# Kernel tuning notes

Measured on AMD Instinct MI355X. Metric: run time of the kernel, lower is better.

The kernel has to match this reference:

```python
import jax, jax.numpy as jnp
import numpy as np

N_STATE = 16
PNAMES = ['in_w', 'conv_w', 'conv_b', 'xproj_w', 'dt_w', 'dt_b', 'A_log', 'D', 'ln_g', 'ln_b', 'out_w']


def _ss2d_params(key, dm, K):
    di = 2 * dm                       # expand = 2
    dr = (dm + 15) // 16              # dt_rank = ceil(d_model/16)
    ks = jax.random.split(key, 6)
    s = lambda k, shape, sc: jax.random.normal(k, shape, jnp.float32) * sc
    cshape = (di, 1, 3, 3) if K == 4 else (di, 1, 3)   # depthwise conv kernel
    return {
        'in_w': s(ks[0], (2 * di, dm), dm ** -0.5),
        'conv_w': s(ks[1], cshape, 0.3),
        'conv_b': jnp.zeros((di,), jnp.float32),
        'xproj_w': s(ks[2], (K, dr + 2 * N_STATE, di), di ** -0.5),
        'dt_w': s(ks[3], (K, di, dr), dr ** -0.5),
        'dt_b': s(ks[4], (K, di), 0.1),
        'A_log': jnp.log(jnp.arange(1, N_STATE + 1, dtype=jnp.float32)) * jnp.ones((K, di, N_STATE), jnp.float32),
        'D': jnp.ones((K, di), jnp.float32),
        'ln_g': jnp.ones((di,), jnp.float32),
        'ln_b': jnp.zeros((di,), jnp.float32),
        'out_w': s(ks[5], (dm, di), di ** -0.5),
    }


def _ln(x, g, b, eps=1e-5):
    m = jnp.mean(x, -1, keepdims=True)
    v = jnp.mean((x - m) ** 2, -1, keepdims=True)
    return (x - m) * jax.lax.rsqrt(v + eps) * g + b


def _scan_branches(xs, p):
    # xs: (B, K, di, L) -- selective scan along L for each direction k
    dr = p['dt_w'].shape[-1]
    x_dbl = jnp.einsum('bkdl,kcd->bkcl', xs, p['xproj_w'])
    dts, Bs, Cs = jnp.split(x_dbl, [dr, dr + N_STATE], axis=2)
    delta = jax.nn.softplus(jnp.einsum('bkrl,kdr->bkdl', dts, p['dt_w']) + p['dt_b'][None, :, :, None])
    A = -jnp.exp(p['A_log'])                               # (K, di, N)
    dA = jnp.exp(jnp.einsum('bkdl,kdn->lbkdn', delta, A))  # time-major for scan
    dBu = jnp.einsum('bkdl,bknl,bkdl->lbkdn', delta, Bs, xs)

    def step(h, io):
        a, bu = io
        h = a * h + bu
        return h, h

    h0 = jnp.zeros(dA.shape[1:], xs.dtype)
    _, hs = jax.lax.scan(step, h0, (dA, dBu))              # (L, B, K, di, N)
    y = jnp.einsum('lbkdn,bknl->bkdl', hs, Cs)
    return y + xs * p['D'][None, :, :, None]


def _ss2d_2d(x, p):
    # VMamba SS2D: x (B, H, W, dm) -> (B, H, W, dm), 4 scan directions
    xz = jnp.einsum('bhwc,ec->bhwe', x, p['in_w'])
    xin, z = jnp.split(xz, 2, -1)
    u = xin.transpose(0, 3, 1, 2)
    u = jax.lax.conv_general_dilated(u, p['conv_w'], (1, 1), 'SAME',
        dimension_numbers=('NCHW', 'OIHW', 'NCHW'), feature_group_count=u.shape[1])
    u = jax.nn.silu(u + p['conv_b'][None, :, None, None])
    Bb, di, H, W = u.shape
    L = H * W
    xf = u.reshape(Bb, di, L)                              # row-major
    xt = u.transpose(0, 1, 3, 2).reshape(Bb, di, L)        # col-major
    xs = jnp.stack([xf, xt, xf[..., ::-1], xt[..., ::-1]], 1)
    ys = _scan_branches(xs, p)                             # (B, 4, di, L)
    y0 = ys[:, 0]
    y2 = ys[:, 2][..., ::-1]
    y1 = ys[:, 1].reshape(Bb, di, W, H).transpose(0, 1, 3, 2).reshape(Bb, di, L)
    y3 = ys[:, 3][..., ::-1].reshape(Bb, di, W, H).transpose(0, 1, 3, 2).reshape(Bb, di, L)
    y = (y0 + y1 + y2 + y3).transpose(0, 2, 1).reshape(Bb, H, W, di)
    y = _ln(y, p['ln_g'], p['ln_b']) * jax.nn.silu(z)
    return jnp.einsum('bhwe,ce->bhwc', y, p['out_w'])


def _ss2d_1d(x, p):
    # SS2D_xb fuse block: x (B, L, dm) -> (B, L, dm), bidirectional 1D scan
    xz = jnp.einsum('blc,ec->ble', x, p['in_w'])
    xin, z = jnp.split(xz, 2, -1)
    u = xin.transpose(0, 2, 1)
    u = jax.lax.conv_general_dilated(u, p['conv_w'], (1,), 'SAME',
        dimension_numbers=('NCH', 'OIH', 'NCH'), feature_group_count=u.shape[1])
    u = jax.nn.silu(u + p['conv_b'][None, :, None])
    xs = jnp.stack([u, u[..., ::-1]], 1)                   # K = 2
    ys = _scan_branches(xs, p)
    y = (ys[:, 0] + ys[:, 1][..., ::-1]).transpose(0, 2, 1)
    y = _ln(y, p['ln_g'], p['ln_b']) * jax.nn.silu(z)
    return jnp.einsum('ble,ce->blc', y, p['out_w'])


def _bridge(C1, C2, C3, p1, p2, p3, pf, n1_g, n1_b):
    y1 = _ss2d_2d(C1.transpose(0, 2, 3, 1), p1).transpose(0, 3, 1, 2)
    y2 = _ss2d_2d(C2.transpose(0, 2, 3, 1), p2).transpose(0, 3, 1, 2)
    y3 = _ss2d_2d(C3.transpose(0, 2, 3, 1), p3).transpose(0, 3, 1, 2)
    B_, C, H, W = y1.shape                                 # C=24, H=W=112
    # faithful RAW reshapes (no permute), exactly as the torch source does
    F1 = y1.reshape(B_, H * W, C)
    F2 = y2.reshape(B_, H * W // 2, C)
    F3 = y3.reshape(B_, H * W // 4, C)
    F = jnp.concatenate([F1, F2, F3], axis=1)              # (B, 21952, 24)
    F = F + _ss2d_1d(_ln(F, n1_g, n1_b), pf)               # dropout = identity (eval)
    o1 = F[:, :12544, :].reshape(B_, C, H, W)
    o2 = F[:, 12544:18816, :].reshape(B_, C * 2, H // 2, W // 2)
    o3 = F[:, 18816:, :].reshape(B_, C * 4, H // 4, W // 4)
    return (o1, o2, o3)


def setup_inputs() -> dict:
    key = jax.random.key(0)
    ks = jax.random.split(key, 7)
    inp = {
        'C1': jax.random.normal(ks[0], (1, 24, 112, 112), jnp.float32),
        'C2': jax.random.normal(ks[1], (1, 48, 56, 56), jnp.float32),
        'C3': jax.random.normal(ks[2], (1, 96, 28, 28), jnp.float32),
    }
    for pfx, dm, K, kk in [('m1', 24, 4, ks[3]), ('m2', 48, 4, ks[4]), ('m3', 96, 4, ks[5]), ('fz', 24, 2, ks[6])]:
        p = _ss2d_params(kk, dm, K)
        for n in PNAMES:
            inp[pfx + '_' + n] = p[n]
    inp['n1_g'] = jnp.ones((24,), jnp.float32)
    inp['n1_b'] = jnp.zeros((24,), jnp.float32)
    return inp


def reference(C1, C2, C3, m1_in_w, m1_conv_w, m1_conv_b, m1_xproj_w, m1_dt_w, m1_dt_b, m1_A_log, m1_D, m1_ln_g, m1_ln_b, m1_out_w, m2_in_w, m2_conv_w, m2_conv_b, m2_xproj_w, m2_dt_w, m2_dt_b, m2_A_log, m2_D, m2_ln_g, m2_ln_b, m2_out_w, m3_in_w, m3_conv_w, m3_conv_b, m3_xproj_w, m3_dt_w, m3_dt_b, m3_A_log, m3_D, m3_ln_g, m3_ln_b, m3_out_w, fz_in_w, fz_conv_w, fz_conv_b, fz_xproj_w, fz_dt_w, fz_dt_b, fz_A_log, fz_D, fz_ln_g, fz_ln_b, fz_out_w, n1_g, n1_b):
    p1 = dict(zip(PNAMES, (m1_in_w, m1_conv_w, m1_conv_b, m1_xproj_w, m1_dt_w, m1_dt_b, m1_A_log, m1_D, m1_ln_g, m1_ln_b, m1_out_w)))
    p2 = dict(zip(PNAMES, (m2_in_w, m2_conv_w, m2_conv_b, m2_xproj_w, m2_dt_w, m2_dt_b, m2_A_log, m2_D, m2_ln_g, m2_ln_b, m2_out_w)))
    p3 = dict(zip(PNAMES, (m3_in_w, m3_conv_w, m3_conv_b, m3_xproj_w, m3_dt_w, m3_dt_b, m3_A_log, m3_D, m3_ln_g, m3_ln_b, m3_out_w)))
    pf = dict(zip(PNAMES, (fz_in_w, fz_conv_w, fz_conv_b, fz_xproj_w, fz_dt_w, fz_dt_b, fz_A_log, fz_D, fz_ln_g, fz_ln_b, fz_out_w)))
    return _bridge(C1, C2, C3, p1, p2, p3, pf, n1_g, n1_b)
```

## Files before the change

kernel.cpp:

```cpp
#include <hip/hip_runtime.h>
#include <hip/hip_bf16.h>
#include <hip/hip_fp16.h>

#define NST 16
#define L2E 1.4426950408889634f

typedef const void* inp;
typedef __half h16;

struct Job {
  inp Cin;
  inp in_w, conv_w, conv_b, xproj_w, dt_w, dt_b, A_log, D, ln_g, ln_b, out_w;
  h16 *u_pre, *z, *u, *delta, *Bs, *Cs, *yg;
  h16 *Hc;
  float *yacc, *Wc, *bc, *Ssum, *A2t, *F0out;
  float *outF; const float* resid;
  const int* aflg;
  int dm, di, dr, K, H, W, L, NCH, CLEN, is2d, TL, CG, PT, cinf;
};
struct Jobs { Job j[4]; int n; const int* dtf; };

__device__ __forceinline__ float ldw(inp p, size_t i, int f32){
  return f32 ? ((const float*)p)[i]
             : __bfloat162float(((const __hip_bfloat16*)p)[i]);
}
__device__ __forceinline__ float hf(const h16* p, size_t i){ return __half2float(p[i]); }
__device__ __forceinline__ float sigm(float x){ return 1.0f/(1.0f + __expf(-x)); }
__device__ __forceinline__ float silu_(float x){ return x * sigm(x); }
__device__ __forceinline__ float softp(float x){ return (x > 20.0f) ? x : __logf(1.0f + __expf(x)); }

__device__ __forceinline__ int map_pos(const Job& J, int k, int l){
  int rev   = J.is2d ? (k >= 2) : (k == 1);
  int trans = J.is2d ? (k & 1) : 0;
  int sl = rev ? (J.L - 1 - l) : l;
  return trans ? ((sl % J.H)*J.W + sl / J.H) : sl;
}

union F4H { float4 f; __half2 h[4]; };

__device__ __forceinline__ void ld16v(const h16* p, float* o){
  const float4* q = (const float4*)p;
  F4H a, b; a.f = q[0]; b.f = q[1];
  #pragma unroll
  for (int i = 0; i < 4; i++){ float2 x = __half22float2(a.h[i]); o[2*i] = x.x; o[2*i+1] = x.y; }
  #pragma unroll
  for (int i = 0; i < 4; i++){ float2 x = __half22float2(b.h[i]); o[8+2*i] = x.x; o[8+2*i+1] = x.y; }
}

__device__ __forceinline__ void ld8v(const h16* p, float* o){
  F4H a; a.f = *(const float4*)p;
  #pragma unroll
  for (int i = 0; i < 4; i++){ float2 x = __half22float2(a.h[i]); o[2*i] = x.x; o[2*i+1] = x.y; }
}


__global__ void k_detect(const unsigned* D1, int* flag){
  if (threadIdx.x == 0 && blockIdx.x == 0)
    flag[0] = (D1[0] == 0x3F800000u) ? 1 : 0;
}

__global__ void k_wcomb(Jobs js){
  int f32 = *js.dtf;
  int b = blockIdx.x;
  for (int m = 0; m < js.n; m++){
    const Job& J = js.j[m];
    int CC = J.di + 2*NST;
    int CC2 = CC + NST;
    int tot = J.K * CC2 * J.di;
    int nb = (tot + 255) >> 8;
    if (b < nb){
      int t = (b << 8) + (int)threadIdx.x;
      if (t < tot){
        int d = t % J.di; int r = t / J.di; int cout = r % CC2; int k = r / CC2;
        if (cout < J.di){
          float v = 0.0f;
          for (int rr = 0; rr < J.dr; rr++)
            v += ldw(J.dt_w, (size_t)(k*J.di + cout)*J.dr + rr, f32) *
                 ldw(J.xproj_w, (size_t)(k*(J.dr + 2*NST) + rr)*J.di + d, f32);
          J.Wc[(size_t)(k*CC + cout)*J.di + d] = v;
          if (d == 0) J.bc[k*CC + cout] = ldw(J.dt_b, k*J.di + cout, f32);
        } else if (cout < CC){
          int nn = cout - J.di;
          J.Wc[(size_t)(k*CC + cout)*J.di + d] =
            ldw(J.xproj_w, (size_t)(k*(J.dr + 2*NST) + J.dr + nn)*J.di + d, f32);
          if (d == 0) J.bc[k*CC + cout] = 0.0f;
        } else {
          int nn = cout - CC;
          J.A2t[(size_t)(k*NST + nn)*J.di + d] =
            -L2E*__expf(ldw(J.A_log, ((size_t)(k*J.di + d) << 4) + nn, f32));
        }
      }
      return;
    }
    b -= nb;
  }
}

__global__ void k_chkA(Jobs js, int* afl){
  int m = blockIdx.x;
  if (m >= js.n) return;
  const Job& J = js.j[m];
  __shared__ int ok;
  if (threadIdx.x == 0) ok = 1;
  __syncthreads();
  int tot = J.K * NST * J.di;
  int bad = 0;
  for (int t = threadIdx.x; t < tot; t += 256){
    int d = t % J.di; int r = t / J.di; int n = r % NST; int k = r / NST;
    float base = J.A2t[(size_t)(k*NST + 0)*J.di + d];
    float v    = J.A2t[(size_t)(k*NST + n)*J.di + d];
    float expect = (float)(n+1)*base;
    if (fabsf(v - expect) > 1e-4f*fabsf(expect) + 1e-6f) bad = 1;
  }
  if (bad) ok = 0;
  __syncthreads();
  if (threadIdx.x == 0) afl[m] = ok;
}

__global__ void k_inproj(Jobs js){
  int f32 = *js.dtf;
  int b = blockIdx.x;
  for (int m = 0; m < js.n; m++){
    const Job& J = js.j[m];
    int tot = 2*J.di*J.L;
    int nb = (tot + 255) >> 8;
    if (b < nb){
      int cf = J.cinf ? 1 : f32;
      int t = (b << 8) + (int)threadIdx.x;
      if (t < tot){
        int p = t % J.L; int e = t / J.L;
        float acc;
        if (cf && f32){
          const float* Ci = (const float*)J.Cin;
          const float4* w4 = (const float4*)((const float*)J.in_w + (size_t)e*J.dm);
          float a0 = 0.f, a1 = 0.f, a2 = 0.f, a3 = 0.f;
          int n4 = J.dm >> 2;
          for (int c4 = 0; c4 < n4; c4++){
            float4 w = w4[c4];
            int c = c4 << 2;
            a0 = fmaf(Ci[(size_t)(c+0)*J.L + p], w.x, a0);
            a1 = fmaf(Ci[(size_t)(c+1)*J.L + p], w.y, a1);
            a2 = fmaf(Ci[(size_t)(c+2)*J.L + p], w.z, a2);
            a3 = fmaf(Ci[(size_t)(c+3)*J.L + p], w.w, a3);
          }
          acc = (a0+a1)+(a2+a3);
        } else {
          float a0 = 0.f, a1 = 0.f, a2 = 0.f, a3 = 0.f;
          for (int c = 0; c < J.dm; c += 4){
            a0 = fmaf(ldw(J.Cin, (size_t)(c+0)*J.L + p, cf), ldw(J.in_w, (size_t)e*J.dm + c+0, f32), a0);
            a1 = fmaf(ldw(J.Cin, (size_t)(c+1)*J.L + p, cf), ldw(J.in_w, (size_t)e*J.dm + c+1, f32), a1);
            a2 = fmaf(ldw(J.Cin, (size_t)(c+2)*J.L + p, cf), ldw(J.in_w, (size_t)e*J.dm + c+2, f32), a2);
            a3 = fmaf(ldw(J.Cin, (size_t)(c+3)*J.L + p, cf), ldw(J.in_w, (size_t)e*J.dm + c+3, f32), a3);
          }
          acc = (a0+a1)+(a2+a3);
        }
        if (e < J.di) J.u_pre[(size_t)p*J.di + e] = __float2half(acc);
        else          J.z[(size_t)p*J.di + (e - J.di)] = __float2half(acc);
      }
      return;
    }
    b -= nb;
  }
}

__global__ void k_conv(Jobs js){
  int f32 = *js.dtf;
  int b = blockIdx.x;
  for (int m = 0; m < js.n; m++){
    const Job& J = js.j[m];
    int tot = J.L * J.di;
    int nb = (tot + 255) >> 8;
    if (b < nb){
      int t = (b << 8) + (int)threadIdx.x;
      if (t < tot){
        int d = t % J.di; int p = t / J.di;
        float acc = ldw(J.conv_b, d, f32);
        if (J.is2d){
          int h = p / J.W, w = p % J.W;
          for (int kh = 0; kh < 3; kh++){
            int hh = h + kh - 1;
            if ((unsigned)hh < (unsigned)J.H){
              for (int kw = 0; kw < 3; kw++){
                int ww = w + kw - 1;
                if ((unsigned)ww < (unsigned)J.W)
                  acc += ldw(J.conv_w, d*9 + kh*3 + kw, f32) * hf(J.u_pre, (size_t)(hh*J.W + ww)*J.di + d);
              }
            }
          }
        } else {
          for (int kk = 0; kk < 3; kk++){
            int pp = p + kk - 1;
            if ((unsigned)pp < (unsigned)J.L)
              acc += ldw(J.conv_w, d*3 + kk, f32) * hf(J.u_pre, (size_t)pp*J.di + d);
          }
        }
        J.u[(size_t)p*J.di + d] = __float2half(silu_(acc));
      }
      return;
    }
    b -= nb;
  }
}

__global__ void k_deltaBC(Jobs js){
  extern __shared__ float xt[];
  int b = blockIdx.x;
  for (int m = 0; m < js.n; m++){
    const Job& J = js.j[m];
    int TL = J.TL;
    int ntile = (J.L + TL - 1)/TL;
    int nb = J.K * ntile;
    if (b < nb){
      int k = b / ntile, tile = b % ntile;
      int l0 = tile * TL;
      int stride = J.di + 4;
      int d8n = J.di >> 3;
      int VE = TL * d8n;
      for (int idx = threadIdx.x; idx < VE; idx += 256){
        int ll = idx / d8n, d8 = idx % d8n;
        int l = l0 + ll;
        float o[8];
        if (l < J.L){
          ld8v(J.u + (size_t)map_pos(J, k, l)*J.di + (d8 << 3), o);
        } else {
          for (int i = 0; i < 8; i++) o[i] = 0.0f;
        }
        float4* dst = (float4*)(xt + ll*stride + (d8 << 3));
        dst[0] = make_float4(o[0],o[1],o[2],o[3]);
        dst[1] = make_float4(o[4],o[5],o[6],o[7]);
      }
      if (k == 0){
        int lend = l0 + TL; if (lend > J.L) lend = J.L;
        int zt = (lend - l0)*J.di >> 2;
        float4* yz = (float4*)(J.yacc + (size_t)l0*J.di);
        for (int idx = threadIdx.x; idx < zt; idx += 256)
          yz[idx] = make_float4(0.f,0.f,0.f,0.f);
      }
      __syncthreads();
      int CC = J.di + 2*NST;
      int c4n = CC >> 2;
      int NL4 = TL >> 2;
      int items = NL4 * c4n;
      int n4 = J.di >> 2;
      for (int item = threadIdx.x; item < items; item += 256){
        int l4 = item % NL4;
        int cbase = (item / NL4) << 2;
        const float4* w0 = (const float4*)(J.Wc + (size_t)(k*CC + cbase+0)*J.di);
        const float4* w1 = (const float4*)(J.Wc + (size_t)(k*CC + cbase+1)*J.di);
        const float4* w2 = (const float4*)(J.Wc + (size_t)(k*CC + cbase+2)*J.di);
        const float4* w3 = (const float4*)(J.Wc + (size_t)(k*CC + cbase+3)*J.di);
        const float4* x0 = (const float4*)(xt + (l4 + 0*NL4)*stride);
        const float4* x1 = (const float4*)(xt + (l4 + 1*NL4)*stride);
        const float4* x2 = (const float4*)(xt + (l4 + 2*NL4)*stride);
        const float4* x3 = (const float4*)(xt + (l4 + 3*NL4)*stride);
        float acc[4][4];
        #pragma unroll
        for (int j = 0; j < 4; j++){
          acc[j][0]=0.f; acc[j][1]=0.f; acc[j][2]=0.f; acc[j][3]=0.f;
        }
        #pragma unroll 4
        for (int d4 = 0; d4 < n4; d4++){
          float4 W0 = w0[d4], W1 = w1[d4], W2 = w2[d4], W3 = w3[d4];
          float4 X0 = x0[d4], X1 = x1[d4], X2 = x2[d4], X3 = x3[d4];
          #define DOT4(a,X,W) { a = fmaf(X.x,W.x,a); a = fmaf(X.y,W.y,a); a = fmaf(X.z,W.z,a); a = fmaf(X.w,W.w,a); }
          DOT4(acc[0][0],X0,W0) DOT4(acc[0][1],X0,W1) DOT4(acc[0][2],X0,W2) DOT4(acc[0][3],X0,W3)
          DOT4(acc[1][0],X1,W0) DOT4(acc[1][1],X1,W1) DOT4(acc[1][2],X1,W2) DOT4(acc[1][3],X1,W3)
          DOT4(acc[2][0],X2,W0) DOT4(acc[2][1],X2,W1) DOT4(acc[2][2],X2,W2) DOT4(acc[2][3],X2,W3)
          DOT4(acc[3][0],X3,W0) DOT4(acc[3][1],X3,W1) DOT4(acc[3][2],X3,W2) DOT4(acc[3][3],X3,W3)
          #undef DOT4
        }
        float b0 = J.bc[k*CC + cbase+0], b1 = J.bc[k*CC + cbase+1];
        float b2 = J.bc[k*CC + cbase+2], b3 = J.bc[k*CC + cbase+3];
        #pragma unroll
        for (int j = 0; j < 4; j++){
          int l = l0 + l4 + NL4*j;
          if (l >= J.L) continue;
          float av[4] = {acc[j][0]+b0, acc[j][1]+b1, acc[j][2]+b2, acc[j][3]+b3};
          #pragma unroll
          for (int i = 0; i < 4; i++){
            int cout = cbase + i; float v = av[i];
            if (cout < J.di)            J.delta[((size_t)k*J.L + l)*J.di + cout] = __float2half(softp(v));
            else if (cout < J.di + NST) J.Bs[((size_t)k*J.L + l)*NST + (cout - J.di)] = __float2half(v);
            else                        J.Cs[((size_t)k*J.L + l)*NST + (cout - J.di - NST)] = __float2half(v);
          }
        }
      }
      return;
    }
    b -= nb;
  }
}

#define STEPRQ { if (rev){ if(--rm < 0){ rm = J.H - 1; qd--; } } else { if(++rm == J.H){ rm = 0; qd++; } } }

#define HUPD_GEN(S, DX, B) { \
  _Pragma("unroll") \
  for (int n = 0; n < NST; n++) h[n] = fmaf(exp2f((S) * A2[n]), h[n], (DX) * (B)[n]); }
#define HUPD_POW(S, DX, B) { \
  float q = exp2f((S) * A2[0]); float a = q; \
  h[0] = fmaf(a, h[0], (DX) * (B)[0]); \
  _Pragma("unroll") \
  for (int n = 1; n < NST; n++){ a *= q; h[n] = fmaf(a, h[n], (DX) * (B)[n]); } }
#define HUPDY_GEN(S, DX, B, C, Y) { \
  _Pragma("unroll") \
  for (int n = 0; n < NST; n++){ h[n] = fmaf(exp2f((S) * A2[n]), h[n], (DX) * (B)[n]); (Y) = fmaf(h[n], (C)[n], (Y)); } }
#define HUPDY_POW(S, DX, B, C, Y) { \
  float q = exp2f((S) * A2[0]); float a = q; \
  h[0] = fmaf(a, h[0], (DX) * (B)[0]); (Y) = fmaf(h[0], (C)[0], (Y)); \
  _Pragma("unroll") \
  for (int n = 1; n < NST; n++){ a *= q; h[n] = fmaf(a, h[n], (DX) * (B)[n]); (Y) = fmaf(h[n], (C)[n], (Y)); } }

__global__ __launch_bounds__(64) void k_passA(Jobs js){
  int b = blockIdx.x;
  for (int m = 0; m < js.n; m++){
    const Job& J = js.j[m];
    int DG = (J.di + 63) >> 6;
    int nb = J.K * J.NCH * DG;
    if (b < nb){
      int afl = *J.aflg;
      int k = b / (J.NCH * DG);
      int r = b % (J.NCH * DG);
      int chunk = r / DG, dg = r % DG;
      int d = (dg << 6) + (int)threadIdx.x;
      if (d >= J.di) return;
      int c0 = chunk * J.CLEN;
      int c1 = c0 + J.CLEN; if (c1 > J.L) c1 = J.L;
      if (c0 >= J.L){
        size_t sb0 = (size_t)(k*J.NCH + chunk);
        J.Ssum[sb0*J.di + d] = 0.0f;
        #pragma unroll
        for (int n = 0; n < NST; n++) J.Hc[(sb0*NST + n)*J.di + d] = __float2half(0.0f);
        return;
      }
      float A2[NST];
      #pragma unroll
      for (int n = 0; n < NST; n++) A2[n] = J.A2t[(size_t)(k*NST + n)*J.di + d];
      float h[NST];
      #pragma unroll
      for (int n = 0; n < NST; n++) h[n] = 0.0f;
      float ss = 0.0f;
      int rev   = J.is2d ? (k >= 2) : (k == 1);
      int trans = J.is2d ? (k & 1) : 0;
      int rm = 0, qd = 0;
      if (trans){
        int sl0 = rev ? (J.L - 1 - c0) : c0;
        qd = sl0 / J.H; rm = sl0 % J.H;
      }
      const h16* dlt   = J.delta + ((size_t)k*J.L)*J.di + d;
      const h16* Bbase = J.Bs + ((size_t)k*J.L)*NST;
      int l = c0;
      while (l < c1){
        int rem = c1 - l;
        int pos0, pos1 = 0;
        if (trans){ pos0 = rm*J.W + qd; STEPRQ; }
        else pos0 = rev ? (J.L - 1 - l) : l;
        float s0 = hf(dlt, (size_t)l*J.di);
        float x0 = hf(J.u, (size_t)pos0*J.di + d);
        float B0[NST]; ld16v(Bbase + (size_t)l*NST, B0);
        float s1 = 0.f, x1 = 0.f; float B1[NST];
        if (rem > 1){
          if (trans){ pos1 = rm*J.W + qd; STEPRQ; }
          else pos1 = rev ? (J.L - 1 - (l+1)) : (l+1);
          s1 = hf(dlt, (size_t)(l+1)*J.di);
          x1 = hf(J.u, (size_t)pos1*J.di + d);
          ld16v(Bbase + (size_t)(l+1)*NST, B1);
        }
        float dx0 = s0 * x0; ss += s0;
        if (afl){ HUPD_POW(s0, dx0, B0) } else { HUPD_GEN(s0, dx0, B0) }
        if (rem > 1){
          float dx1 = s1 * x1; ss += s1;
          if (afl){ HUPD_POW(s1, dx1, B1) } else { HUPD_GEN(s1, dx1, B1) }
        }
        l += 2;
      }
      size_t sb = (size_t)(k*J.NCH + chunk);
      J.Ssum[sb*J.di + d] = ss;
      #pragma unroll
      for (int n = 0; n < NST; n++)
        J.Hc[(sb*NST + n)*J.di + d] = __float2half(h[n]);
      return;
    }
    b -= nb;
  }
}

__global__ void k_passB(Jobs js){
  __shared__ float sP[16*17], sH[16*17], pH[16*17];
  int b = blockIdx.x;
  for (int m = 0; m < js.n; m++){
    const Job& J = js.j[m];
    int DT = J.di >> 4;
    int nb = J.K * NST * DT;
    if (b < nb){
      int k  = b / (NST*DT);
      int r  = b % (NST*DT);
      int n  = r / DT;
      int dt = r % DT;
      int sid = (int)threadIdx.x >> 4;
      int dd  = (int)threadIdx.x & 15;
      int d = dt*16 + dd;
      int SL = J.NCH >> 4;
      int c0 = sid*SL, c1 = c0 + SL;
      float An = J.A2t[(size_t)(k*NST + n)*J.di + d];
      float a = 1.0f, hagg = 0.0f;
      for (int c = c0; c < c1; c++){
        size_t rowb = (size_t)(k*J.NCH + c);
        float P = exp2f(An * J.Ssum[rowb*J.di + d]);
        float hc = hf(J.Hc, (rowb*NST + n)*J.di + d);
        hagg = fmaf(P, hagg, hc);
        a *= P;
      }
      sP[sid*17+dd] = a; sH[sid*17+dd] = hagg;
      __syncthreads();
      if (sid == 0){
        float X = 0.0f;
        for (int s = 0; s < 16; s++){
          pH[s*17+dd] = X;
          X = fmaf(sP[s*17+dd], X, sH[s*17+dd]);
        }
      }
      __syncthreads();
      float Hp = pH[sid*17+dd];
      size_t rowb0 = (size_t)(k*J.NCH + c0);
      float ss_nx = J.Ssum[rowb0*J.di + d];
      float hc_nx = hf(J.Hc, (rowb0*NST + n)*J.di + d);
      for (int c = c0; c < c1; c++){
        float ss = ss_nx, hc = hc_nx;
        size_t idx = ((size_t)(k*J.NCH + c)*NST + n)*J.di + d;
        if (c + 1 < c1){
          size_t rowb = (size_t)(k*J.NCH + c + 1);
          ss_nx = J.Ssum[rowb*J.di + d];
          hc_nx = hf(J.Hc, (rowb*NST + n)*J.di + d);
        }
        float P = exp2f(An * ss);
        J.Hc[idx] = __float2half(Hp);
        Hp = fmaf(P, Hp, hc);
      }
      return;
    }
    b -= nb;
  }
}

__global__ __launch_bounds__(64) void k_passC(Jobs js){
  int f32 = *js.dtf;
  int b = blockIdx.x;
  for (int m = 0; m < js.n; m++){
    const Job& J = js.j[m];
    int DG = (J.di + 63) >> 6;
    int nb = J.K * J.NCH * DG;
    if (b < nb){
      int afl = *J.aflg;
      int k = b / (J.NCH * DG);
      int r = b % (J.NCH * DG);
      int chunk = r / DG, dg = r % DG;
      int d = (dg << 6) + (int)threadIdx.x;
      if (d >= J.di) return;
      int c0 = chunk * J.CLEN;
      int c1 = c0 + J.CLEN; if (c1 > J.L) c1 = J.L;
      if (c0 >= J.L) return;
      float A2[NST];
      #pragma unroll
      for (int n = 0; n < NST; n++) A2[n] = J.A2t[(size_t)(k*NST + n)*J.di + d];
      float h[NST];
      size_t sb = (size_t)(k*J.NCH + chunk);
      #pragma unroll
      for (int n = 0; n < NST; n++) h[n] = hf(J.Hc, (sb*NST + n)*J.di + d);
      float Dd = ldw(J.D, k*J.di + d, f32);
      int rev   = J.is2d ? (k >= 2) : (k == 1);
      int trans = J.is2d ? (k & 1) : 0;
      int rm = 0, qd = 0;
      if (trans){
        int sl0 = rev ? (J.L - 1 - c0) : c0;
        qd = sl0 / J.H; rm = sl0 % J.H;
      }
      const h16* dlt   = J.delta + ((size_t)k*J.L)*J.di + d;
      const h16* Bbase = J.Bs + ((size_t)k*J.L)*NST;
      const h16* Cbase = J.Cs + ((size_t)k*J.L)*NST;
      int l = c0;
      while (l < c1){
        int rem = c1 - l;
        int pos0, pos1 = 0;
        if (trans){ pos0 = rm*J.W + qd; STEPRQ; }
        else pos0 = rev ? (J.L - 1 - l) : l;
        float s0 = hf(dlt, (size_t)l*J.di);
        float x0 = hf(J.u, (size_t)pos0*J.di + d);
        float B0[NST], C0[NST];
        ld16v(Bbase + (size_t)l*NST, B0);
        ld16v(Cbase + (size_t)l*NST, C0);
        float s1 = 0.f, x1 = 0.f; float B1[NST], C1[NST];
        if (rem > 1){
          if (trans){ pos1 = rm*J.W + qd; STEPRQ; }
          else pos1 = rev ? (J.L - 1 - (l+1)) : (l+1);
          s1 = hf(dlt, (size_t)(l+1)*J.di);
          x1 = hf(J.u, (size_t)pos1*J.di + d);
          ld16v(Bbase + (size_t)(l+1)*NST, B1);
          ld16v(Cbase + (size_t)(l+1)*NST, C1);
        }
        float dx0 = s0 * x0;
        float y0 = 0.0f;
        if (afl){ HUPDY_POW(s0, dx0, B0, C0, y0) } else { HUPDY_GEN(s0, dx0, B0, C0, y0) }
        y0 = fmaf(Dd, x0, y0);
        atomicAdd(&J.yacc[(size_t)pos0*J.di + d], y0);
        if (rem > 1){
          float dx1 = s1 * x1;
          float y1 = 0.0f;
          if (afl){ HUPDY_POW(s1, dx1, B1, C1, y1) } else { HUPDY_GEN(s1, dx1, B1, C1, y1) }
          y1 = fmaf(Dd, x1, y1);
          atomicAdd(&J.yacc[(size_t)pos1*J.di + d], y1);
        }
        l += 2;
      }
      return;
    }
    b -= nb;
  }
}

__global__ void k_merge(Jobs js){
  extern __shared__ float sm[];
  const Job& J = js.j[0];
  int f32 = *js.dtf;
  int di = J.di, PT = J.PT;
  int st = di + 1, st2 = di + 2;
  int p0 = blockIdx.x * PT;
  int rows = J.L - p0; if (rows > PT) rows = PT;
  float* ya = sm;
  h16*   zz = (h16*)(sm + (size_t)PT*st);
  float* mres = (float*)(zz + (size_t)PT*st2);
  float* owT = mres + 2*PT;
  int tot = rows*di;
  for (int idx = threadIdx.x; idx < tot; idx += 256){
    int r = idx / di, d = idx % di;
    ya[r*st + d] = J.yacc[(size_t)p0*di + idx];
    zz[r*st2 + d] = J.z[(size_t)p0*di + idx];
  }
  if (J.outF){
    for (int idx = threadIdx.x; idx < J.dm*di; idx += 256){
      int c = idx / di, e = idx % di;
      owT[e*25 + c] = ldw(J.out_w, (size_t)c*di + e, f32);
    }
  }
  __syncthreads();
  int wid = (int)threadIdx.x >> 6, lane = (int)threadIdx.x & 63;
  for (int r = wid; r < rows; r += 4){
    float s = 0.0f, s2 = 0.0f;
    for (int d = lane; d < di; d += 64){
      float v = ya[r*st + d];
      s += v; s2 = fmaf(v, v, s2);
    }
    for (int o = 32; o > 0; o >>= 1){
      s  += __shfl_down(s, o);
      s2 += __shfl_down(s2, o);
    }
    if (lane == 0){
      float mean = s / di;
      float var = s2/di - mean*mean;
      mres[r] = mean;
      mres[PT + r] = rsqrtf(var + 1e-5f);
    }
  }
  __syncthreads();
  if (J.outF){
    {
      int r = (int)threadIdx.x & (PT - 1);
      int dgrp = (int)threadIdx.x / PT;
      int G = 256 / PT;
      if (r < rows){
        float mean = mres[r], rs = mres[PT + r];
        for (int d = dgrp; d < di; d += G){
          float ln = (ya[r*st + d] - mean)*rs*ldw(J.ln_g, d, f32) + ldw(J.ln_b, d, f32);
          ya[r*st + d] = ln * silu_(__half2float(zz[r*st2 + d]));
        }
      }
    }
    __syncthreads();
    for (int idx = threadIdx.x; idx < rows*J.dm; idx += 256){
      int r = idx / J.dm, c = idx % J.dm;
      const float* lr = ya + r*st;
      float acc = 0.0f;
      for (int e = 0; e < di; e += 8){
        #pragma unroll
        for (int j = 0; j < 8; j++)
          acc = fmaf(lr[e+j], owT[(e+j)*25 + c], acc);
      }
      size_t o = (size_t)(p0 + r)*J.dm + c;
      J.outF[o] = J.resid[o] + acc;
    }
  } else {
    int r = (int)threadIdx.x & (PT - 1);
    int dgrp = (int)threadIdx.x / PT;
    int G = 256 / PT;
    if (r < rows){
      float mean = mres[r], rs = mres[PT + r];
      int p = p0 + r;
      for (int d = dgrp; d < di; d += G){
        float ln = (ya[r*st + d] - mean)*rs*ldw(J.ln_g, d, f32) + ldw(J.ln_b, d, f32);
        J.yg[(size_t)d*J.L + p] = __float2half(ln * silu_(__half2float(zz[r*st2 + d])));
      }
    }
  }
}

__global__ void k_outproj(Jobs js){
  int f32 = *js.dtf;
  int b = blockIdx.x;
  for (int m = 0; m < js.n; m++){
    const Job& J = js.j[m];
    int tot = J.dm * J.L;
    int nb = (tot + 255) >> 8;
    if (b < nb){
      int t = (b << 8) + (int)threadIdx.x;
      if (t < tot){
        int p = t % J.L; int c = t / J.L;
        float acc = 0.0f;
        for (int e = 0; e < J.di; e += 8){
          #pragma unroll
          for (int j = 0; j < 8; j++)
            acc = fmaf(hf(J.yg, (size_t)(e+j)*J.L + p),
                       ldw(J.out_w, (size_t)c*J.di + e + j, f32), acc);
        }
        J.F0out[(size_t)c*J.L + p] = acc;
      }
      return;
    }
    b -= nb;
  }
}

__global__ void k_lnrows(const float* F0, inp g, inp bb, float* xt_, int L, int C, const int* dtf){
  __shared__ float sm[256*25];
  int f32 = *dtf;
  int p0 = blockIdx.x * 256;
  int rows = L - p0; if (rows > 256) rows = 256;
  int tot = rows * C;
  for (int idx = threadIdx.x; idx < tot; idx += 256){
    int r = idx / C, c = idx % C;
    sm[r*25 + c] = F0[(size_t)p0*C + idx];
  }
  __syncthreads();
  int r = threadIdx.x;
  if (r < rows){
    const float* row = sm + r*25;
    float s = 0.0f;
    for (int c = 0; c < C; c++) s += row[c];
    float mean = s / C;
    float s2 = 0.0f;
    for (int c = 0; c < C; c++){ float t = row[c]-mean; s2 += t*t; }
    float rs = rsqrtf(s2/C + 1e-5f);
    int p = p0 + r;
    for (int c = 0; c < C; c++)
      xt_[(size_t)c*L + p] = (row[c]-mean)*rs*ldw(g,c,f32) + ldw(bb,c,f32);
  }
}

static inline int cdiv_i(int a, int b){ return (a + b - 1)/b; }

extern "C" void kernel_launch(void* const* d_in, const int* in_sizes, int n_in,
                              void* d_out, int out_size, void* d_ws, size_t ws_size,
                              hipStream_t stream){
  (void)in_sizes; (void)n_in; (void)out_size; (void)ws_size;
  char* base = (char*)d_ws;
  size_t off = 0;
  auto alloc = [&](size_t bytes)->char*{
    off = (off + 255) & ~(size_t)255;
    char* p = base + off; off += bytes; return p;
  };

  int*   dtf = (int*)alloc(4);
  int*   afl = (int*)alloc(4*4);
  float* F0  = (float*)alloc(526848u*4);
  float* Wc1 = (float*)alloc(4u*80*48*4);   float* bc1 = (float*)alloc(4u*80*4);
  float* Wc2 = (float*)alloc(4u*128*96*4);  float* bc2 = (float*)alloc(4u*128*4);
  float* Wc3 = (float*)alloc(4u*224*192*4); float* bc3 = (float*)alloc(4u*224*4);
  float* Wcf = (float*)alloc(2u*80*48*4);   float* bcf = (float*)alloc(2u*80*4);
  float* A21 = (float*)alloc(4u*NST*48*4);
  float* A22 = (float*)alloc(4u*NST*96*4);
  float* A23 = (float*)alloc(4u*NST*192*4);
  float* A2f = (float*)alloc(2u*NST*48*4);
  size_t regionA = off;

  auto fill = [&](Job& J, int pbase, inp Cin, int cinf,
                  int dm, int di, int dr, int K, int H, int W, int L,
                  int NCH, int CLEN, int is2d, int TL, int PT,
                  float* Wc, float* bc, float* A2t, float* F0out){
    J.Cin = Cin; J.cinf = cinf;
    J.in_w    = d_in[pbase+0];
    J.conv_w  = d_in[pbase+1];
    J.conv_b  = d_in[pbase+2];
    J.xproj_w = d_in[pbase+3];
    J.dt_w    = d_in[pbase+4];
    J.dt_b    = d_in[pbase+5];
    J.A_log   = d_in[pbase+6];
    J.D       = d_in[pbase+7];
    J.ln_g    = d_in[pbase+8];
    J.ln_b    = d_in[pbase+9];
    J.out_w   = d_in[pbase+10];
    size_t LD = (size_t)L*di;
    J.yacc  = (float*)alloc(LD*4);
    J.u_pre = (h16*)J.yacc;
    J.z     = (h16*)alloc(LD*2);
    J.u     = (h16*)alloc(LD*2);
    J.yg    = J.u;
    J.delta = (h16*)alloc((size_t)K*LD*2);
    J.Bs    = (h16*)alloc((size_t)K*L*NST*2);
    J.Cs    = (h16*)alloc((size_t)K*L*NST*2);
    J.Hc    = (h16*)alloc((size_t)K*NCH*NST*di*2);
    J.Ssum  = (float*)alloc((size_t)K*NCH*di*4);
    J.Wc = Wc; J.bc = bc; J.A2t = A2t; J.F0out = F0out;
    J.outF = nullptr; J.resid = nullptr;
    J.dm=dm; J.di=di; J.dr=dr; J.K=K; J.H=H; J.W=W; J.L=L; J.NCH=NCH; J.CLEN=CLEN;
    J.is2d=is2d; J.TL=TL; J.CG=256/TL; J.PT=PT;
  };

  Jobs js3; js3.n = 3; js3.dtf = dtf;
  fill(js3.j[0],  3, d_in[0], 0, 24,  48, 2, 4, 112, 112, 12544, 512, 25, 1, 64, 32, Wc1, bc1, A21, F0);
  fill(js3.j[1], 14, d_in[1], 0, 48,  96, 3, 4,  56,  56,  3136, 128, 25, 1, 32, 32, Wc2, bc2, A22, F0 + 301056);
  fill(js3.j[2], 25, d_in[2], 0, 96, 192, 6, 4,  28,  28,   784,  32, 25, 1, 16, 16, Wc3, bc3, A23, F0 + 451584);
  js3.j[0].aflg = afl + 0;
  js3.j[1].aflg = afl + 1;
  js3.j[2].aflg = afl + 2;

  off = regionA;
  float* xlnT = (float*)alloc(24u*21952*4);
  Jobs js1; js1.n = 1; js1.dtf = dtf;
  fill(js1.j[0], 36, nullptr, 1, 24, 48, 2, 2, 21952, 1, 21952, 1024, 22, 0, 64, 32, Wcf, bcf, A2f, nullptr);
  js1.j[0].Cin = xlnT;
  js1.j[0].aflg = afl + 3;
  js1.j[0].outF = (float*)d_out;
  js1.j[0].resid = F0;

  Jobs js4; js4.n = 4; js4.dtf = dtf;
  js4.j[0] = js3.j[0]; js4.j[1] = js3.j[1]; js4.j[2] = js3.j[2]; js4.j[3] = js1.j[0];

  auto grids = [&](const Jobs& js, int which)->int{
    int g = 0;
    for (int m = 0; m < js.n; m++){
      const Job& J = js.j[m];
      switch (which){
        case 0: g += cdiv_i(J.K*(J.di+3*NST)*J.di, 256); break;
        case 1: g += cdiv_i(2*J.di*J.L, 256); break;
        case 2: g += cdiv_i(J.L*J.di, 256); break;
        case 4: g += J.K * J.NCH * cdiv_i(J.di, 64); break;
        case 5: g += J.K * NST * (J.di >> 4); break;
        case 7: g += cdiv_i(J.dm*J.L, 256); break;
      }
    }
    return g;
  };

  auto launch_dbc = [&](const Job& Jin){
    Jobs one; one.n = 1; one.dtf = dtf; one.j[0] = Jin;
    const Job& J = one.j[0];
    int grid = J.K * cdiv_i(J.L, J.TL);
    int shm = J.TL*(J.di+4)*4;
    k_deltaBC<<<grid, 256, shm, stream>>>(one);
  };
  auto launch_merge = [&](const Job& Jin){
    Jobs one; one.n = 1; one.dtf = dtf; one.j[0] = Jin;
    const Job& J = one.j[0];
    int grid = cdiv_i(J.L, J.PT);
    int shm = J.PT*(J.di+1)*4 + J.PT*(J.di+2)*2 + 2*J.PT*4 + (J.outF ? 48*25*4 : 0);
    k_merge<<<grid, 256, shm, stream>>>(one);
  };

  k_detect <<<1, 64, 0, stream>>>((const unsigned*)d_in[10], dtf);

  k_wcomb  <<<grids(js4,0), 256, 0, stream>>>(js4);
  k_chkA   <<<4, 256, 0, stream>>>(js4, afl);
  k_inproj <<<grids(js3,1), 256, 0, stream>>>(js3);
  k_conv   <<<grids(js3,2), 256, 0, stream>>>(js3);
  for (int m = 0; m < 3; m++) launch_dbc(js3.j[m]);
  k_passA  <<<grids(js3,4),  64, 0, stream>>>(js3);
  k_passB  <<<grids(js3,5), 256, 0, stream>>>(js3);
  k_passC  <<<grids(js3,4),  64, 0, stream>>>(js3);
  for (int m = 0; m < 3; m++) launch_merge(js3.j[m]);
  k_outproj<<<grids(js3,7), 256, 0, stream>>>(js3);

  k_lnrows <<<cdiv_i(21952,256), 256, 0, stream>>>(F0, d_in[47], d_in[48], xlnT, 21952, 24, dtf);
  k_inproj <<<grids(js1,1), 256, 0, stream>>>(js1);
  k_conv   <<<grids(js1,2), 256, 0, stream>>>(js1);
  launch_dbc(js1.j[0]);
  k_passA  <<<grids(js1,4),  64, 0, stream>>>(js1);
  k_passB  <<<grids(js1,5), 256, 0, stream>>>(js1);
  k_passC  <<<grids(js1,4),  64, 0, stream>>>(js1);
  launch_merge(js1.j[0]);
}
```

Baseline: 549.7 us.

## Rework chunked scan passes: 4 waves per block, power-tree decay, prefetch, more chunks

The chunked selective-scan passes A and C now pack four 64-lane waves per 256-thread block, and the chunk count is doubled so each chunk is about half as long. In the A_log==log(n) fast path, the 16 sequential multiplies that build the decay powers become a shallow power tree. Loads for the next two timesteps are prefetched as raw half/float4 registers, so memory latency overlaps the recurrence arithmetic. More chunks gives more parallelism but makes pass B's inter-chunk combine longer, and prefetching raises register pressure.

```diff
diff --git a/kernel.cpp b/kernel.cpp
--- a/kernel.cpp
+++ b/kernel.cpp
@@ -51,6 +51,14 @@
   F4H a; a.f = *(const float4*)p;
   #pragma unroll
   for (int i = 0; i < 4; i++){ float2 x = __half22float2(a.h[i]); o[2*i] = x.x; o[2*i+1] = x.y; }
+}
+
+__device__ __forceinline__ void cvt16(float4 a4, float4 b4, float* o){
+  F4H a, b; a.f = a4; b.f = b4;
+  #pragma unroll
+  for (int i = 0; i < 4; i++){ float2 x = __half22float2(a.h[i]); o[2*i] = x.x; o[2*i+1] = x.y; }
+  #pragma unroll
+  for (int i = 0; i < 4; i++){ float2 x = __half22float2(b.h[i]); o[8+2*i] = x.x; o[8+2*i+1] = x.y; }
 }
 
 
@@ -296,45 +304,55 @@
 #define HUPD_GEN(S, DX, B) { \
   _Pragma("unroll") \
   for (int n = 0; n < NST; n++) h[n] = fmaf(exp2f((S) * A2[n]), h[n], (DX) * (B)[n]); }
-#define HUPD_POW(S, DX, B) { \
-  float q = exp2f((S) * A2[0]); float a = q; \
-  h[0] = fmaf(a, h[0], (DX) * (B)[0]); \
-  _Pragma("unroll") \
-  for (int n = 1; n < NST; n++){ a *= q; h[n] = fmaf(a, h[n], (DX) * (B)[n]); } }
 #define HUPDY_GEN(S, DX, B, C, Y) { \
   _Pragma("unroll") \
   for (int n = 0; n < NST; n++){ h[n] = fmaf(exp2f((S) * A2[n]), h[n], (DX) * (B)[n]); (Y) = fmaf(h[n], (C)[n], (Y)); } }
+
+#define POWTREE(Q, P) \
+  float P[NST]; \
+  P[0]=(Q); P[1]=P[0]*P[0]; P[2]=P[1]*P[0]; P[3]=P[1]*P[1]; \
+  P[4]=P[3]*P[0]; P[5]=P[3]*P[1]; P[6]=P[3]*P[2]; P[7]=P[3]*P[3]; \
+  P[8]=P[7]*P[0]; P[9]=P[7]*P[1]; P[10]=P[7]*P[2]; P[11]=P[7]*P[3]; \
+  P[12]=P[7]*P[4]; P[13]=P[7]*P[5]; P[14]=P[7]*P[6]; P[15]=P[7]*P[7];
+
+#define HUPD_POW(S, DX, B) { \
+  float q_ = exp2f((S) * A0); \
+  POWTREE(q_, Pw) \
+  _Pragma("unroll") \
+  for (int n = 0; n < NST; n++) h[n] = fmaf(Pw[n], h[n], (DX) * (B)[n]); }
 #define HUPDY_POW(S, DX, B, C, Y) { \
-  float q = exp2f((S) * A2[0]); float a = q; \
-  h[0] = fmaf(a, h[0], (DX) * (B)[0]); (Y) = fmaf(h[0], (C)[0], (Y)); \
+  float q_ = exp2f((S) * A0); \
+  POWTREE(q_, Pw) \
   _Pragma("unroll") \
-  for (int n = 1; n < NST; n++){ a *= q; h[n] = fmaf(a, h[n], (DX) * (B)[n]); (Y) = fmaf(h[n], (C)[n], (Y)); } }
-
-__global__ __launch_bounds__(64) void k_passA(Jobs js){
+  for (int n = 0; n < NST; n++){ h[n] = fmaf(Pw[n], h[n], (DX) * (B)[n]); (Y) = fmaf(h[n], (C)[n], (Y)); } }
+
+__global__ __launch_bounds__(256) void k_passA(Jobs js){
   int b = blockIdx.x;
+  int wid = (int)threadIdx.x >> 6;
+  int lane = (int)threadIdx.x & 63;
   for (int m = 0; m < js.n; m++){
     const Job& J = js.j[m];
     int DG = (J.di + 63) >> 6;
-    int nb = J.K * J.NCH * DG;
+    int units = J.K * J.NCH * DG;
+    int nb = (units + 3) >> 2;
     if (b < nb){
+      int uu = (b << 2) + wid;
+      if (uu >= units) return;
       int afl = *J.aflg;
-      int k = b / (J.NCH * DG);
-      int r = b % (J.NCH * DG);
+      int k = uu / (J.NCH * DG);
+      int r = uu % (J.NCH * DG);
       int chunk = r / DG, dg = r % DG;
-      int d = (dg << 6) + (int)threadIdx.x;
+      int d = (dg << 6) + lane;
       if (d >= J.di) return;
       int c0 = chunk * J.CLEN;
       int c1 = c0 + J.CLEN; if (c1 > J.L) c1 = J.L;
+      size_t sb = (size_t)(k*J.NCH + chunk);
       if (c0 >= J.L){
-        size_t sb0 = (size_t)(k*J.NCH + chunk);
-        J.Ssum[sb0*J.di + d] = 0.0f;
+        J.Ssum[sb*J.di + d] = 0.0f;
         #pragma unroll
-        for (int n = 0; n < NST; n++) J.Hc[(sb0*NST + n)*J.di + d] = __float2half(0.0f);
+        for (int n = 0; n < NST; n++) J.Hc[(sb*NST + n)*J.di + d] = __float2half(0.0f);
         return;
       }
-      float A2[NST];
-      #pragma unroll
-      for (int n = 0; n < NST; n++) A2[n] = J.A2t[(size_t)(k*NST + n)*J.di + d];
       float h[NST];
       #pragma unroll
       for (int n = 0; n < NST; n++) h[n] = 0.0f;
@@ -346,34 +364,74 @@
         int sl0 = rev ? (J.L - 1 - c0) : c0;
         qd = sl0 / J.H; rm = sl0 % J.H;
       }
-      const h16* dlt   = J.delta + ((size_t)k*J.L)*J.di + d;
-      const h16* Bbase = J.Bs + ((size_t)k*J.L)*NST;
-      int l = c0;
-      while (l < c1){
-        int rem = c1 - l;
-        int pos0, pos1 = 0;
-        if (trans){ pos0 = rm*J.W + qd; STEPRQ; }
-        else pos0 = rev ? (J.L - 1 - l) : l;
-        float s0 = hf(dlt, (size_t)l*J.di);
-        float x0 = hf(J.u, (size_t)pos0*J.di + d);
-        float B0[NST]; ld16v(Bbase + (size_t)l*NST, B0);
-        float s1 = 0.f, x1 = 0.f; float B1[NST];
-        if (rem > 1){
-          if (trans){ pos1 = rm*J.W + qd; STEPRQ; }
-          else pos1 = rev ? (J.L - 1 - (l+1)) : (l+1);
-          s1 = hf(dlt, (size_t)(l+1)*J.di);
-          x1 = hf(J.u, (size_t)pos1*J.di + d);
-          ld16v(Bbase + (size_t)(l+1)*NST, B1);
-        }
-        float dx0 = s0 * x0; ss += s0;
-        if (afl){ HUPD_POW(s0, dx0, B0) } else { HUPD_GEN(s0, dx0, B0) }
-        if (rem > 1){
-          float dx1 = s1 * x1; ss += s1;
-          if (afl){ HUPD_POW(s1, dx1, B1) } else { HUPD_GEN(s1, dx1, B1) }
-        }
-        l += 2;
-      }
-      size_t sb = (size_t)(k*J.NCH + chunk);
+      const h16* dlt = J.delta + ((size_t)k*J.L)*J.di + d;
+      const h16* Bb  = J.Bs + ((size_t)k*J.L)*NST;
+      if (afl){
+        float A0 = J.A2t[(size_t)(k*NST)*J.di + d];
+        int l = c0;
+        int pos0;
+        h16 s0h, s1h, x0h, x1h;
+        float4 B0a, B0b, B1a, B1b;
+        if (trans){ pos0 = rm*J.W + qd; STEPRQ; } else pos0 = rev ? (J.L-1-l) : l;
+        s0h = dlt[(size_t)l*J.di];
+        x0h = J.u[(size_t)pos0*J.di + d];
+        { const float4* bp = (const float4*)(Bb + (size_t)l*NST); B0a = bp[0]; B0b = bp[1]; }
+        s1h = s0h; x1h = x0h; B1a = B0a; B1b = B0b;
+        if (l + 1 < c1){
+          int pos1;
+          if (trans){ pos1 = rm*J.W + qd; STEPRQ; } else pos1 = rev ? (J.L-2-l) : (l+1);
+          s1h = dlt[(size_t)(l+1)*J.di];
+          x1h = J.u[(size_t)pos1*J.di + d];
+          const float4* bq = (const float4*)(Bb + (size_t)(l+1)*NST); B1a = bq[0]; B1b = bq[1];
+        }
+        while (l < c1){
+          int ln = l + 2;
+          h16 ns0 = s0h, ns1 = s1h, nx0 = x0h, nx1 = x1h;
+          float4 nB0a = B0a, nB0b = B0b, nB1a = B1a, nB1b = B1b;
+          if (ln < c1){
+            int np0;
+            if (trans){ np0 = rm*J.W + qd; STEPRQ; } else np0 = rev ? (J.L-1-ln) : ln;
+            ns0 = dlt[(size_t)ln*J.di];
+            nx0 = J.u[(size_t)np0*J.di + d];
+            const float4* bp = (const float4*)(Bb + (size_t)ln*NST); nB0a = bp[0]; nB0b = bp[1];
+            if (ln + 1 < c1){
+              int np1;
+              if (trans){ np1 = rm*J.W + qd; STEPRQ; } else np1 = rev ? (J.L-2-ln) : (ln+1);
+              ns1 = dlt[(size_t)(ln+1)*J.di];
+              nx1 = J.u[(size_t)np1*J.di + d];
+              const float4* bq = (const float4*)(Bb + (size_t)(ln+1)*NST); nB1a = bq[0]; nB1b = bq[1];
+            }
+          }
+          {
+            float s0 = __half2float(s0h), x0 = __half2float(x0h);
+            float B0[NST]; cvt16(B0a, B0b, B0);
+            float dx0 = s0 * x0; ss += s0;
+            HUPD_POW(s0, dx0, B0)
+            if (l + 1 < c1){
+              float s1 = __half2float(s1h), x1 = __half2float(x1h);
+              float B1[NST]; cvt16(B1a, B1b, B1);
+              float dx1 = s1 * x1; ss += s1;
+              HUPD_POW(s1, dx1, B1)
+            }
+          }
+          l = ln;
+          s0h = ns0; s1h = ns1; x0h = nx0; x1h = nx1;
+          B0a = nB0a; B0b = nB0b; B1a = nB1a; B1b = nB1b;
+        }
+      } else {
+        float A2[NST];
+        #pragma unroll
+        for (int n = 0; n < NST; n++) A2[n] = J.A2t[(size_t)(k*NST + n)*J.di + d];
+        for (int l = c0; l < c1; l++){
+          int pos;
+          if (trans){ pos = rm*J.W + qd; STEPRQ; } else pos = rev ? (J.L-1-l) : l;
+          float s0 = hf(dlt, (size_t)l*J.di);
+          float x0 = hf(J.u, (size_t)pos*J.di + d);
+          float B0[NST]; ld16v(Bb + (size_t)l*NST, B0);
+          float dx0 = s0 * x0; ss += s0;
+          HUPD_GEN(s0, dx0, B0)
+        }
+      }
       J.Ssum[sb*J.di + d] = ss;
       #pragma unroll
       for (int n = 0; n < NST; n++)
@@ -442,26 +500,28 @@
   }
 }
 
-__global__ __launch_bounds__(64) void k_passC(Jobs js){
+__global__ __launch_bounds__(256) void k_passC(Jobs js){
   int f32 = *js.dtf;
   int b = blockIdx.x;
+  int wid = (int)threadIdx.x >> 6;
+  int lane = (int)threadIdx.x & 63;
   for (int m = 0; m < js.n; m++){
     const Job& J = js.j[m];
     int DG = (J.di + 63) >> 6;
-    int nb = J.K * J.NCH * DG;
+    int units = J.K * J.NCH * DG;
+    int nb = (units + 3) >> 2;
     if (b < nb){
+      int uu = (b << 2) + wid;
+      if (uu >= units) return;
       int afl = *J.aflg;
-      int k = b / (J.NCH * DG);
-      int r = b % (J.NCH * DG);
+      int k = uu / (J.NCH * DG);
+      int r = uu % (J.NCH * DG);
       int chunk = r / DG, dg = r % DG;
-      int d = (dg << 6) + (int)threadIdx.x;
+      int d = (dg << 6) + lane;
       if (d >= J.di) return;
       int c0 = chunk * J.CLEN;
       int c1 = c0 + J.CLEN; if (c1 > J.L) c1 = J.L;
       if (c0 >= J.L) return;
-      float A2[NST];
-      #pragma unroll
-      for (int n = 0; n < NST; n++) A2[n] = J.A2t[(size_t)(k*NST + n)*J.di + d];
       float h[NST];
       size_t sb = (size_t)(k*J.NCH + chunk);
       #pragma unroll
@@ -474,42 +534,89 @@
         int sl0 = rev ? (J.L - 1 - c0) : c0;
         qd = sl0 / J.H; rm = sl0 % J.H;
       }
-      const h16* dlt   = J.delta + ((size_t)k*J.L)*J.di + d;
-      const h16* Bbase = J.Bs + ((size_t)k*J.L)*NST;
-      const h16* Cbase = J.Cs + ((size_t)k*J.L)*NST;
-      int l = c0;
-      while (l < c1){
-        int rem = c1 - l;
+      const h16* dlt = J.delta + ((size_t)k*J.L)*J.di + d;
+      const h16* Bb  = J.Bs + ((size_t)k*J.L)*NST;
+      const h16* Cb  = J.Cs + ((size_t)k*J.L)*NST;
+      if (afl){
+        float A0 = J.A2t[(size_t)(k*NST)*J.di + d];
+        int l = c0;
         int pos0, pos1 = 0;
-        if (trans){ pos0 = rm*J.W + qd; STEPRQ; }
-        else pos0 = rev ? (J.L - 1 - l) : l;
-        float s0 = hf(dlt, (size_t)l*J.di);
-        float x0 = hf(J.u, (size_t)pos0*J.di + d);
-        float B0[NST], C0[NST];
-        ld16v(Bbase + (size_t)l*NST, B0);
-        ld16v(Cbase + (size_t)l*NST, C0);
-        float s1 = 0.f, x1 = 0.f; float B1[NST], C1[NST];
-        if (rem > 1){
-          if (trans){ pos1 = rm*J.W + qd; STEPRQ; }
-          else pos1 = rev ? (J.L - 1 - (l+1)) : (l+1);
-          s1 = hf(dlt, (size_t)(l+1)*J.di);
-          x1 = hf(J.u, (size_t)pos1*J.di + d);
-          ld16v(Bbase + (size_t)(l+1)*NST, B1);
-          ld16v(Cbase + (size_t)(l+1)*NST, C1);
-        }
-        float dx0 = s0 * x0;
-        float y0 = 0.0f;
-        if (afl){ HUPDY_POW(s0, dx0, B0, C0, y0) } else { HUPDY_GEN(s0, dx0, B0, C0, y0) }
-        y0 = fmaf(Dd, x0, y0);
-        atomicAdd(&J.yacc[(size_t)pos0*J.di + d], y0);
-        if (rem > 1){
-          float dx1 = s1 * x1;
-          float y1 = 0.0f;
-          if (afl){ HUPDY_POW(s1, dx1, B1, C1, y1) } else { HUPDY_GEN(s1, dx1, B1, C1, y1) }
-          y1 = fmaf(Dd, x1, y1);
-          atomicAdd(&J.yacc[(size_t)pos1*J.di + d], y1);
-        }
-        l += 2;
+        h16 s0h, s1h, x0h, x1h;
+        float4 B0a, B0b, B1a, B1b, C0a, C0b, C1a, C1b;
+        if (trans){ pos0 = rm*J.W + qd; STEPRQ; } else pos0 = rev ? (J.L-1-l) : l;
+        s0h = dlt[(size_t)l*J.di];
+        x0h = J.u[(size_t)pos0*J.di + d];
+        { const float4* bp = (const float4*)(Bb + (size_t)l*NST); B0a = bp[0]; B0b = bp[1];
+          const float4* cp = (const float4*)(Cb + (size_t)l*NST); C0a = cp[0]; C0b = cp[1]; }
+        s1h = s0h; x1h = x0h; B1a = B0a; B1b = B0b; C1a = C0a; C1b = C0b;
+        if (l + 1 < c1){
+          if (trans){ pos1 = rm*J.W + qd; STEPRQ; } else pos1 = rev ? (J.L-2-l) : (l+1);
+          s1h = dlt[(size_t)(l+1)*J.di];
+          x1h = J.u[(size_t)pos1*J.di + d];
+          const float4* bq = (const float4*)(Bb + (size_t)(l+1)*NST); B1a = bq[0]; B1b = bq[1];
+          const float4* cq = (const float4*)(Cb + (size_t)(l+1)*NST); C1a = cq[0]; C1b = cq[1];
+        }
+        while (l < c1){
+          int ln = l + 2;
+          int np0 = pos0, np1 = pos1;
+          h16 ns0 = s0h, ns1 = s1h, nx0 = x0h, nx1 = x1h;
+          float4 nB0a = B0a, nB0b = B0b, nB1a = B1a, nB1b = B1b;
+          float4 nC0a = C0a, nC0b = C0b, nC1a = C1a, nC1b = C1b;
+          if (ln < c1){
+            if (trans){ np0 = rm*J.W + qd; STEPRQ; } else np0 = rev ? (J.L-1-ln) : ln;
+            ns0 = dlt[(size_t)ln*J.di];
+            nx0 = J.u[(size_t)np0*J.di + d];
+            { const float4* bp = (const float4*)(Bb + (size_t)ln*NST); nB0a = bp[0]; nB0b = bp[1];
+              const float4* cp = (const float4*)(Cb + (size_t)ln*NST); nC0a = cp[0]; nC0b = cp[1]; }
+            if (ln + 1 < c1){
+              if (trans){ np1 = rm*J.W + qd; STEPRQ; } else np1 = rev ? (J.L-2-ln) : (ln+1);
+              ns1 = dlt[(size_t)(ln+1)*J.di];
+              nx1 = J.u[(size_t)np1*J.di + d];
+              const float4* bq = (const float4*)(Bb + (size_t)(ln+1)*NST); nB1a = bq[0]; nB1b = bq[1];
+              const float4* cq = (const float4*)(Cb + (size_t)(ln+1)*NST); nC1a = cq[0]; nC1b = cq[1];
+            }
+          }
+          {
+            float s0 = __half2float(s0h), x0 = __half2float(x0h);
+            float B0[NST], C0[NST]; cvt16(B0a, B0b, B0); cvt16(C0a, C0b, C0);
+            float dx0 = s0 * x0;
+            float y0 = 0.0f;
+            HUPDY_POW(s0, dx0, B0, C0, y0)
+            y0 = fmaf(Dd, x0, y0);
+            atomicAdd(&J.yacc[(size_t)pos0*J.di + d], y0);
+            if (l + 1 < c1){
+              float s1 = __half2float(s1h), x1 = __half2float(x1h);
+              float B1[NST], C1[NST]; cvt16(B1a, B1b, B1); cvt16(C1a, C1b, C1);
+              float dx1 = s1 * x1;
+              float y1 = 0.0f;
+              HUPDY_POW(s1, dx1, B1, C1, y1)
+              y1 = fmaf(Dd, x1, y1);
+              atomicAdd(&J.yacc[(size_t)pos1*J.di + d], y1);
+            }
+          }
+          l = ln; pos0 = np0; pos1 = np1;
+          s0h = ns0; s1h = ns1; x0h = nx0; x1h = nx1;
+          B0a = nB0a; B0b = nB0b; B1a = nB1a; B1b = nB1b;
+          C0a = nC0a; C0b = nC0b; C1a = nC1a; C1b = nC1b;
+        }
+      } else {
+        float A2[NST];
+        #pragma unroll
+        for (int n = 0; n < NST; n++) A2[n] = J.A2t[(size_t)(k*NST + n)*J.di + d];
+        for (int l = c0; l < c1; l++){
+          int pos;
+          if (trans){ pos = rm*J.W + qd; STEPRQ; } else pos = rev ? (J.L-1-l) : l;
+          float s0 = hf(dlt, (size_t)l*J.di);
+          float x0 = hf(J.u, (size_t)pos*J.di + d);
+          float B0[NST], C0[NST];
+          ld16v(Bb + (size_t)l*NST, B0);
+          ld16v(Cb + (size_t)l*NST, C0);
+          float dx0 = s0 * x0;
+          float y0 = 0.0f;
+          HUPDY_GEN(s0, dx0, B0, C0, y0)
+          y0 = fmaf(Dd, x0, y0);
+          atomicAdd(&J.yacc[(size_t)pos*J.di + d], y0);
+        }
       }
       return;
     }
@@ -714,9 +821,9 @@
   };
 
   Jobs js3; js3.n = 3; js3.dtf = dtf;
-  fill(js3.j[0],  3, d_in[0], 0, 24,  48, 2, 4, 112, 112, 12544, 512, 25, 1, 64, 32, Wc1, bc1, A21, F0);
-  fill(js3.j[1], 14, d_in[1], 0, 48,  96, 3, 4,  56,  56,  3136, 128, 25, 1, 32, 32, Wc2, bc2, A22, F0 + 301056);
-  fill(js3.j[2], 25, d_in[2], 0, 96, 192, 6, 4,  28,  28,   784,  32, 25, 1, 16, 16, Wc3, bc3, A23, F0 + 451584);
+  fill(js3.j[0],  3, d_in[0], 0, 24,  48, 2, 4, 112, 112, 12544, 1024, 13, 1, 64, 32, Wc1, bc1, A21, F0);
+  fill(js3.j[1], 14, d_in[1], 0, 48,  96, 3, 4,  56,  56,  3136,  256, 13, 1, 32, 32, Wc2, bc2, A22, F0 + 301056);
+  fill(js3.j[2], 25, d_in[2], 0, 96, 192, 6, 4,  28,  28,   784,   64, 13, 1, 16, 16, Wc3, bc3, A23, F0 + 451584);
   js3.j[0].aflg = afl + 0;
   js3.j[1].aflg = afl + 1;
   js3.j[2].aflg = afl + 2;
@@ -724,7 +831,7 @@
   off = regionA;
   float* xlnT = (float*)alloc(24u*21952*4);
   Jobs js1; js1.n = 1; js1.dtf = dtf;
-  fill(js1.j[0], 36, nullptr, 1, 24, 48, 2, 2, 21952, 1, 21952, 1024, 22, 0, 64, 32, Wcf, bcf, A2f, nullptr);
+  fill(js1.j[0], 36, nullptr, 1, 24, 48, 2, 2, 21952, 1, 21952, 2048, 11, 0, 64, 32, Wcf, bcf, A2f, nullptr);
   js1.j[0].Cin = xlnT;
   js1.j[0].aflg = afl + 3;
   js1.j[0].outF = (float*)d_out;
@@ -741,7 +848,7 @@
         case 0: g += cdiv_i(J.K*(J.di+3*NST)*J.di, 256); break;
         case 1: g += cdiv_i(2*J.di*J.L, 256); break;
         case 2: g += cdiv_i(J.L*J.di, 256); break;
-        case 4: g += J.K * J.NCH * cdiv_i(J.di, 64); break;
+        case 4: g += cdiv_i(J.K * J.NCH * cdiv_i(J.di, 64), 4); break;
         case 5: g += J.K * NST * (J.di >> 4); break;
         case 7: g += cdiv_i(J.dm*J.L, 256); break;
       }
@@ -771,9 +878,9 @@
   k_inproj <<<grids(js3,1), 256, 0, stream>>>(js3);
   k_conv   <<<grids(js3,2), 256, 0, stream>>>(js3);
   for (int m = 0; m < 3; m++) launch_dbc(js3.j[m]);
-  k_passA  <<<grids(js3,4),  64, 0, stream>>>(js3);
+  k_passA  <<<grids(js3,4), 256, 0, stream>>>(js3);
   k_passB  <<<grids(js3,5), 256, 0, stream>>>(js3);
-  k_passC  <<<grids(js3,4),  64, 0, stream>>>(js3);
+  k_passC  <<<grids(js3,4), 256, 0, stream>>>(js3);
   for (int m = 0; m < 3; m++) launch_merge(js3.j[m]);
   k_outproj<<<grids(js3,7), 256, 0, stream>>>(js3);
 
@@ -781,8 +888,8 @@
   k_inproj <<<grids(js1,1), 256, 0, stream>>>(js1);
   k_conv   <<<grids(js1,2), 256, 0, stream>>>(js1);
   launch_dbc(js1.j[0]);
-  k_passA  <<<grids(js1,4),  64, 0, stream>>>(js1);
+  k_passA  <<<grids(js1,4), 256, 0, stream>>>(js1);
   k_passB  <<<grids(js1,5), 256, 0, stream>>>(js1);
-  k_passC  <<<grids(js1,4),  64, 0, stream>>>(js1);
+  k_passC  <<<grids(js1,4), 256, 0, stream>>>(js1);
   launch_merge(js1.j[0]);
 }
```

Result: slower. 594.3 us (+8.1%).
